# Optimization experiments

Measured on AMD Instinct MI355X. Metric: run time of the kernel, lower is better.

## Reference

```python
import math
import jax, jax.numpy as jnp
import numpy as np

H_HEADS = 8
K_MAX = 64
MIN_WINDOW = 1.0
SHARPNESS = 5.0


def rmsnorm(x, w, eps=1e-6):
    x32 = x.astype(jnp.float32)
    var = jnp.mean(x32 * x32, axis=-1, keepdims=True)
    return (w * (x32 * jax.lax.rsqrt(var + eps))).astype(x.dtype)


def setup_inputs() -> dict:
    key = jax.random.key(0)
    ks = jax.random.split(key, 12)
    B, L, C = 1, 4096, 256
    H, K = H_HEADS, K_MAX
    s = 0.02
    return {
        "x": jax.random.normal(ks[0], (B, L, C), jnp.float32),
        "window_w": jax.random.normal(ks[1], (C, H), jnp.float32) * s,
        "window_b": jnp.zeros((H,), jnp.float32),
        "window_gamma": jnp.ones((H,), jnp.float32),
        "offset_w": jax.random.normal(ks[2], (C, H), jnp.float32) * s,
        "offset_b": jnp.zeros((H,), jnp.float32),
        "offset_gamma": jnp.ones((H,), jnp.float32),
        "kernel_w": jax.random.normal(ks[3], (C, H * K), jnp.float32) * s,
        "kernel_b": jnp.zeros((H * K,), jnp.float32),
        "kernel_gamma": jnp.ones((H * K,), jnp.float32),
        "v_w": jax.random.normal(ks[4], (C, C), jnp.float32) * (1.0 / math.sqrt(C)),
        "v_b": jnp.zeros((C,), jnp.float32),
        "out_w": jax.random.normal(ks[5], (C, C), jnp.float32) * s,
    }


def reference(x, window_w, window_b, window_gamma, offset_w, offset_b, offset_gamma,
              kernel_w, kernel_b, kernel_gamma, v_w, v_b, out_w):
    B, L, C = x.shape
    H, K = H_HEADS, K_MAX
    D = C // H
    max_window = min(int(math.sqrt(L)), K)
    half = max_window // 2
    max_offset = int(math.sqrt(L))
    N = 2 * half + 1  # num_offsets

    # per-position learned window sizes, center offsets, kernel weights
    window_raw = jax.nn.sigmoid(rmsnorm(x @ window_w + window_b, window_gamma))
    window_sizes = MIN_WINDOW + window_raw * (max_window - MIN_WINDOW)      # [B,L,H]
    center_offsets = jnp.tanh(rmsnorm(x @ offset_w + offset_b, offset_gamma)) * max_offset  # [B,L,H]
    kernel_weights = jax.nn.silu(rmsnorm(x @ kernel_w + kernel_b, kernel_gamma)).reshape(B, L, H, K)
    v = (x @ v_w + v_b).reshape(B, L, H, D)

    local = jnp.arange(-half, half + 1, dtype=x.dtype)                      # [N]
    positions = jnp.arange(L, dtype=x.dtype).reshape(1, L, 1, 1)
    neighbor = positions + center_offsets[..., None] + local.reshape(1, 1, 1, N)  # [B,L,H,N]
    valid = (neighbor >= 0) & (neighbor < L)
    nclamp = jnp.clip(neighbor, 0, L - 1)

    rel = jnp.abs(local).reshape(1, 1, 1, N) / (window_sizes[..., None] / 2 + 1e-6)
    window_mask = jax.nn.sigmoid(SHARPNESS * (1.0 - rel)) * valid.astype(x.dtype)

    # kernel interpolation by relative distance
    kidx = jnp.clip(rel, 0, 1) * (K - 1)
    i_fl = jnp.clip(kidx.astype(jnp.int32), 0, K - 2)                       # [B,L,H,N]
    i_ce = i_fl + 1
    w_ce = kidx - i_fl.astype(x.dtype)
    k_fl = jnp.take_along_axis(kernel_weights, i_fl, axis=-1)
    k_ce = jnp.take_along_axis(kernel_weights, i_ce, axis=-1)
    kernel_interp = k_fl * (1.0 - w_ce) + k_ce * w_ce

    attn = kernel_interp * window_mask
    attn = attn / (jnp.sum(attn, axis=-1, keepdims=True) + 1e-6)            # [B,L,H,N]

    # bilinear gather of values at fractional neighbor positions
    p_fl = jnp.clip(jnp.floor(nclamp).astype(jnp.int32), 0, L - 1)
    p_ce = jnp.clip(p_fl + 1, 0, L - 1)
    frac = nclamp - p_fl.astype(x.dtype)                                    # [B,L,H,N]

    v_bh = v.transpose(0, 2, 1, 3)                                          # [B,H,L,D]
    idx_f = p_fl.transpose(0, 2, 1, 3).reshape(B, H, L * N)
    idx_c = p_ce.transpose(0, 2, 1, 3).reshape(B, H, L * N)
    v_fl = jnp.take_along_axis(v_bh, idx_f[..., None], axis=2).reshape(B, H, L, N, D)
    v_ce = jnp.take_along_axis(v_bh, idx_c[..., None], axis=2).reshape(B, H, L, N, D)
    frac_bh = frac.transpose(0, 2, 1, 3)[..., None]                         # [B,H,L,N,1]
    v_nb = v_fl * (1.0 - frac_bh) + v_ce * frac_bh                          # [B,H,L,N,D]

    attn_bh = attn.transpose(0, 2, 1, 3)                                    # [B,H,L,N]
    out = jnp.einsum('bhln,bhlnd->bhld', attn_bh, v_nb)                     # [B,H,L,D]
    out = out.transpose(0, 2, 1, 3).reshape(B, L, C)
    return jax.nn.silu(out @ out_w)
```

## Files before the change

### kernel.cpp

```cpp
#include <hip/hip_runtime.h>
#include <math.h>

#define L_SEQ 4096
#define C_DIM 256
#define H_HEADS 8
#define K_MAX 64
#define D_HEAD 32
#define HALF_W 32
#define N_OFF 65
#define HK 512
#define PW 768

__device__ __forceinline__ float sigmoidf_(float x) { return 1.0f / (1.0f + expf(-x)); }

__global__ void pack_kernel(const float* __restrict__ kw_w, const float* __restrict__ vw,
                            const float* __restrict__ kb, const float* __restrict__ vb,
                            float* __restrict__ Wcat, float* __restrict__ biascat) {
    const int c = blockIdx.x;
    for (int j = threadIdx.x; j < PW; j += 256) {
        Wcat[c * PW + j] = (j < 512) ? kw_w[c * 512 + j] : vw[c * 256 + (j - 512)];
        if (c == 0) biascat[j] = (j < 512) ? kb[j] : vb[j - 512];
    }
}

__global__ void proj_small_kernel(const float* __restrict__ x,
                                  const float* __restrict__ ww, const float* __restrict__ wb,
                                  const float* __restrict__ wg,
                                  const float* __restrict__ ow, const float* __restrict__ ob,
                                  const float* __restrict__ og,
                                  float* __restrict__ wsizes, float* __restrict__ offs) {
    const int l = blockIdx.x;
    const int lane = threadIdx.x;
    const float* xr = x + l * C_DIM;

    float accw[H_HEADS], acco[H_HEADS];
#pragma unroll
    for (int h = 0; h < H_HEADS; ++h) { accw[h] = 0.0f; acco[h] = 0.0f; }

#pragma unroll
    for (int i = 0; i < C_DIM / 64; ++i) {
        const int c = lane + i * 64;
        const float xv = xr[c];
        const float* wwc = ww + c * H_HEADS;
        const float* owc = ow + c * H_HEADS;
#pragma unroll
        for (int h = 0; h < H_HEADS; ++h) {
            accw[h] = fmaf(xv, wwc[h], accw[h]);
            acco[h] = fmaf(xv, owc[h], acco[h]);
        }
    }
#pragma unroll
    for (int off = 32; off > 0; off >>= 1) {
#pragma unroll
        for (int h = 0; h < H_HEADS; ++h) {
            accw[h] += __shfl_xor(accw[h], off);
            acco[h] += __shfl_xor(acco[h], off);
        }
    }
    if (lane == 0) {
        float zw[H_HEADS], zo[H_HEADS];
        float ssw = 0.0f, sso = 0.0f;
#pragma unroll
        for (int h = 0; h < H_HEADS; ++h) {
            zw[h] = accw[h] + wb[h];
            zo[h] = acco[h] + ob[h];
            ssw += zw[h] * zw[h];
            sso += zo[h] * zo[h];
        }
        const float rw = rsqrtf(ssw / (float)H_HEADS + 1e-6f);
        const float ro = rsqrtf(sso / (float)H_HEADS + 1e-6f);
#pragma unroll
        for (int h = 0; h < H_HEADS; ++h) {
            const float nw = wg[h] * zw[h] * rw;
            const float no = og[h] * zo[h] * ro;
            wsizes[l * H_HEADS + h] = 1.0f + sigmoidf_(nw) * 63.0f;
            offs[l * H_HEADS + h]   = tanhf(no) * 64.0f;
        }
    }
}

template <bool ROUTE>
__global__ void gemm_tiled(const float* __restrict__ A, const float* __restrict__ B,
                           const float* __restrict__ biascat, int ldb,
                           float* __restrict__ out,
                           float* __restrict__ kwbuf, float* __restrict__ vbuf) {
    __shared__ float As[16][68];
    __shared__ float Bs[16][68];

    const int tid = threadIdx.x;
    const int tx = tid & 15;
    const int ty = tid >> 4;
    const int l0 = blockIdx.y * 64;
    const int n0 = blockIdx.x * 64;

    const int am = tid >> 2;
    const int ak = (tid & 3) * 4;
    const int bk = tid >> 4;
    const int bn = (tid & 15) * 4;

    float acc[4][4];
#pragma unroll
    for (int i = 0; i < 4; ++i)
#pragma unroll
        for (int j = 0; j < 4; ++j) acc[i][j] = 0.0f;

    for (int k0 = 0; k0 < C_DIM; k0 += 16) {
        const float4 av = *(const float4*)&A[(l0 + am) * C_DIM + k0 + ak];
        const float4 bv = *(const float4*)&B[(k0 + bk) * ldb + n0 + bn];
        __syncthreads();
        As[ak + 0][am] = av.x;
        As[ak + 1][am] = av.y;
        As[ak + 2][am] = av.z;
        As[ak + 3][am] = av.w;
        *(float4*)&Bs[bk][bn] = bv;
        __syncthreads();
#pragma unroll
        for (int kk = 0; kk < 16; ++kk) {
            const float4 a4 = *(const float4*)&As[kk][ty * 4];
            const float4 b4 = *(const float4*)&Bs[kk][tx * 4];
            const float ar[4] = {a4.x, a4.y, a4.z, a4.w};
            const float br[4] = {b4.x, b4.y, b4.z, b4.w};
#pragma unroll
            for (int i = 0; i < 4; ++i)
#pragma unroll
                for (int j = 0; j < 4; ++j)
                    acc[i][j] = fmaf(ar[i], br[j], acc[i][j]);
        }
    }

    const int g0 = n0 + tx * 4;
    if (ROUTE) {
        const float4 bz = *(const float4*)&biascat[g0];
        float* dst;
        int stride, col;
        if (g0 < 512) { dst = kwbuf; stride = 512; col = g0; }
        else          { dst = vbuf;  stride = 256; col = g0 - 512; }
#pragma unroll
        for (int i = 0; i < 4; ++i) {
            const int row = l0 + ty * 4 + i;
            float4 o;
            o.x = acc[i][0] + bz.x;
            o.y = acc[i][1] + bz.y;
            o.z = acc[i][2] + bz.z;
            o.w = acc[i][3] + bz.w;
            *(float4*)&dst[row * stride + col] = o;
        }
    } else {
#pragma unroll
        for (int i = 0; i < 4; ++i) {
            const int row = l0 + ty * 4 + i;
            float4 o;
            o.x = acc[i][0] * sigmoidf_(acc[i][0]);
            o.y = acc[i][1] * sigmoidf_(acc[i][1]);
            o.z = acc[i][2] * sigmoidf_(acc[i][2]);
            o.w = acc[i][3] * sigmoidf_(acc[i][3]);
            *(float4*)&out[row * C_DIM + g0] = o;
        }
    }
}

__global__ void norm_kw(float* __restrict__ kwbuf, const float* __restrict__ kg) {
    const int l = blockIdx.x;
    const int j = threadIdx.x;
    __shared__ float red[256];
    __shared__ float rs_s;
    float* row = kwbuf + l * HK;
    const float z0 = row[j];
    const float z1 = row[j + 256];

    red[j] = z0 * z0 + z1 * z1;
    __syncthreads();
    for (int s = 128; s > 0; s >>= 1) {
        if (j < s) red[j] += red[j + s];
        __syncthreads();
    }
    if (j == 0) rs_s = rsqrtf(red[0] / (float)HK + 1e-6f);
    __syncthreads();
    const float rs = rs_s;

    const float n0 = kg[j] * z0 * rs;
    const float n1 = kg[j + 256] * z1 * rs;
    row[j]       = n0 * sigmoidf_(n0);
    row[j + 256] = n1 * sigmoidf_(n1);
}

__global__ void conv_kernel(const float* __restrict__ wsizes, const float* __restrict__ offs,
                            const float* __restrict__ kw, const float* __restrict__ v,
                            float* __restrict__ out) {
    const int l = blockIdx.x;
    const int tid = threadIdx.x;

    __shared__ float attn[H_HEADS][N_OFF];
    __shared__ int   pfl[H_HEADS][N_OFF];
    __shared__ float frac[H_HEADS][N_OFF];
    __shared__ float inv_denom[H_HEADS];

    for (int t = tid; t < H_HEADS * N_OFF; t += 256) {
        const int h = t / N_OFF;
        const int n = t - h * N_OFF;
        const float ws  = wsizes[l * H_HEADS + h];
        const float off = offs[l * H_HEADS + h];
        const float local = (float)(n - HALF_W);
        const float neighbor = (float)l + off + local;
        const bool valid = (neighbor >= 0.0f) && (neighbor < (float)L_SEQ);
        const float nc = fminf(fmaxf(neighbor, 0.0f), (float)(L_SEQ - 1));

        const float rel = fabsf(local) / (ws * 0.5f + 1e-6f);
        const float mask = sigmoidf_(5.0f * (1.0f - rel)) * (valid ? 1.0f : 0.0f);

        const float kidx = fminf(rel, 1.0f) * (float)(K_MAX - 1);
        int ifl = (int)kidx;
        ifl = min(ifl, K_MAX - 2);
        const float wce = kidx - (float)ifl;
        const float kf = kw[l * HK + h * K_MAX + ifl];
        const float kc = kw[l * HK + h * K_MAX + ifl + 1];
        attn[h][n] = (kf * (1.0f - wce) + kc * wce) * mask;

        int p = (int)floorf(nc);
        p = min(max(p, 0), L_SEQ - 1);
        pfl[h][n] = p;
        frac[h][n] = nc - (float)p;
    }
    __syncthreads();

    if (tid < H_HEADS) {
        float s = 0.0f;
        for (int n = 0; n < N_OFF; ++n) s += attn[tid][n];
        inv_denom[tid] = 1.0f / (s + 1e-6f);
    }
    __syncthreads();

    const int h = tid >> 5;
    const int d = tid & 31;
    float acc = 0.0f;
    for (int n = 0; n < N_OFF; ++n) {
        const float a = attn[h][n];
        const int   p = pfl[h][n];
        const float f = frac[h][n];
        const int  pc = min(p + 1, L_SEQ - 1);
        const float vf = v[p * C_DIM + h * D_HEAD + d];
        const float vc = v[pc * C_DIM + h * D_HEAD + d];
        acc = fmaf(a, vf + f * (vc - vf), acc);
    }
    out[l * C_DIM + h * D_HEAD + d] = acc * inv_denom[h];
}

extern "C" void kernel_launch(void* const* d_in, const int* in_sizes, int n_in,
                              void* d_out, int out_size, void* d_ws, size_t ws_size,
                              hipStream_t stream) {
    const float* x    = (const float*)d_in[0];
    const float* ww   = (const float*)d_in[1];
    const float* wb   = (const float*)d_in[2];
    const float* wg   = (const float*)d_in[3];
    const float* ow   = (const float*)d_in[4];
    const float* ob   = (const float*)d_in[5];
    const float* og   = (const float*)d_in[6];
    const float* kw_w = (const float*)d_in[7];
    const float* kb   = (const float*)d_in[8];
    const float* kg   = (const float*)d_in[9];
    const float* vw   = (const float*)d_in[10];
    const float* vb   = (const float*)d_in[11];
    const float* outw = (const float*)d_in[12];
    float* y = (float*)d_out;

    float* ws_f     = (float*)d_ws;
    float* convbuf  = ws_f;
    float* Wcat     = ws_f;
    float* biascat  = Wcat + 256 * PW;
    float* kwbuf    = convbuf + L_SEQ * C_DIM;
    float* vbuf     = kwbuf + L_SEQ * HK;
    float* wsizes   = vbuf + L_SEQ * C_DIM;
    float* offs     = wsizes + L_SEQ * H_HEADS;

    pack_kernel<<<256, 256, 0, stream>>>(kw_w, vw, kb, vb, Wcat, biascat);
    proj_small_kernel<<<L_SEQ, 64, 0, stream>>>(x, ww, wb, wg, ow, ob, og, wsizes, offs);
    gemm_tiled<true><<<dim3(PW / 64, L_SEQ / 64), 256, 0, stream>>>(
        x, Wcat, biascat, PW, nullptr, kwbuf, vbuf);
    norm_kw<<<L_SEQ, 256, 0, stream>>>(kwbuf, kg);
    conv_kernel<<<L_SEQ, 256, 0, stream>>>(wsizes, offs, kwbuf, vbuf, convbuf);
    gemm_tiled<false><<<dim3(C_DIM / 64, L_SEQ / 64), 256, 0, stream>>>(
        convbuf, outw, nullptr, C_DIM, y, nullptr, nullptr);
}
```

Baseline: 169.5 us.

## Fuse pack, small projections and kw norm into fewer kernels; prefetch GEMM tiles

Removes the weight-packing kernel by having the projection GEMM read the kernel and value weight matrices directly. The small window/offset projection and the kernel-weight RMSNorm+SiLU are folded into the conv kernel, so the normalized row stays in shared memory instead of being written back and re-read. Both GEMMs register-prefetch the next K tile before computing the current one, and the output GEMM uses 32-row tiles to launch more blocks. This cuts the launch count from six to three and removes intermediate global traffic, at the cost of more shared memory and serial prologue work in the conv block.

```diff
diff --git a/kernel.cpp b/kernel.cpp
--- a/kernel.cpp
+++ b/kernel.cpp
@@ -9,81 +9,13 @@
 #define HALF_W 32
 #define N_OFF 65
 #define HK 512
-#define PW 768
 
 __device__ __forceinline__ float sigmoidf_(float x) { return 1.0f / (1.0f + expf(-x)); }
 
-__global__ void pack_kernel(const float* __restrict__ kw_w, const float* __restrict__ vw,
-                            const float* __restrict__ kb, const float* __restrict__ vb,
-                            float* __restrict__ Wcat, float* __restrict__ biascat) {
-    const int c = blockIdx.x;
-    for (int j = threadIdx.x; j < PW; j += 256) {
-        Wcat[c * PW + j] = (j < 512) ? kw_w[c * 512 + j] : vw[c * 256 + (j - 512)];
-        if (c == 0) biascat[j] = (j < 512) ? kb[j] : vb[j - 512];
-    }
-}
-
-__global__ void proj_small_kernel(const float* __restrict__ x,
-                                  const float* __restrict__ ww, const float* __restrict__ wb,
-                                  const float* __restrict__ wg,
-                                  const float* __restrict__ ow, const float* __restrict__ ob,
-                                  const float* __restrict__ og,
-                                  float* __restrict__ wsizes, float* __restrict__ offs) {
-    const int l = blockIdx.x;
-    const int lane = threadIdx.x;
-    const float* xr = x + l * C_DIM;
-
-    float accw[H_HEADS], acco[H_HEADS];
-#pragma unroll
-    for (int h = 0; h < H_HEADS; ++h) { accw[h] = 0.0f; acco[h] = 0.0f; }
-
-#pragma unroll
-    for (int i = 0; i < C_DIM / 64; ++i) {
-        const int c = lane + i * 64;
-        const float xv = xr[c];
-        const float* wwc = ww + c * H_HEADS;
-        const float* owc = ow + c * H_HEADS;
-#pragma unroll
-        for (int h = 0; h < H_HEADS; ++h) {
-            accw[h] = fmaf(xv, wwc[h], accw[h]);
-            acco[h] = fmaf(xv, owc[h], acco[h]);
-        }
-    }
-#pragma unroll
-    for (int off = 32; off > 0; off >>= 1) {
-#pragma unroll
-        for (int h = 0; h < H_HEADS; ++h) {
-            accw[h] += __shfl_xor(accw[h], off);
-            acco[h] += __shfl_xor(acco[h], off);
-        }
-    }
-    if (lane == 0) {
-        float zw[H_HEADS], zo[H_HEADS];
-        float ssw = 0.0f, sso = 0.0f;
-#pragma unroll
-        for (int h = 0; h < H_HEADS; ++h) {
-            zw[h] = accw[h] + wb[h];
-            zo[h] = acco[h] + ob[h];
-            ssw += zw[h] * zw[h];
-            sso += zo[h] * zo[h];
-        }
-        const float rw = rsqrtf(ssw / (float)H_HEADS + 1e-6f);
-        const float ro = rsqrtf(sso / (float)H_HEADS + 1e-6f);
-#pragma unroll
-        for (int h = 0; h < H_HEADS; ++h) {
-            const float nw = wg[h] * zw[h] * rw;
-            const float no = og[h] * zo[h] * ro;
-            wsizes[l * H_HEADS + h] = 1.0f + sigmoidf_(nw) * 63.0f;
-            offs[l * H_HEADS + h]   = tanhf(no) * 64.0f;
-        }
-    }
-}
-
-template <bool ROUTE>
-__global__ void gemm_tiled(const float* __restrict__ A, const float* __restrict__ B,
-                           const float* __restrict__ biascat, int ldb,
-                           float* __restrict__ out,
-                           float* __restrict__ kwbuf, float* __restrict__ vbuf) {
+__global__ void proj_gemm(const float* __restrict__ A, const float* __restrict__ kw_w,
+                          const float* __restrict__ vw, const float* __restrict__ kb,
+                          const float* __restrict__ vb,
+                          float* __restrict__ kwbuf, float* __restrict__ vbuf) {
     __shared__ float As[16][68];
     __shared__ float Bs[16][68];
 
@@ -98,15 +30,21 @@
     const int bk = tid >> 4;
     const int bn = (tid & 15) * 4;
 
+    const float* Bsrc;
+    int ldb, coff;
+    if (n0 < 512) { Bsrc = kw_w; ldb = 512; coff = n0; }
+    else          { Bsrc = vw;   ldb = 256; coff = n0 - 512; }
+
     float acc[4][4];
 #pragma unroll
     for (int i = 0; i < 4; ++i)
 #pragma unroll
-        for (int j = 0; j < 4; ++j) acc[i][j] = 0.0f;
+        for (int jj = 0; jj < 4; ++jj) acc[i][jj] = 0.0f;
+
+    float4 av = *(const float4*)&A[(l0 + am) * C_DIM + ak];
+    float4 bv = *(const float4*)&Bsrc[bk * ldb + coff + bn];
 
     for (int k0 = 0; k0 < C_DIM; k0 += 16) {
-        const float4 av = *(const float4*)&A[(l0 + am) * C_DIM + k0 + ak];
-        const float4 bv = *(const float4*)&B[(k0 + bk) * ldb + n0 + bn];
         __syncthreads();
         As[ak + 0][am] = av.x;
         As[ak + 1][am] = av.y;
@@ -114,6 +52,10 @@
         As[ak + 3][am] = av.w;
         *(float4*)&Bs[bk][bn] = bv;
         __syncthreads();
+        if (k0 + 16 < C_DIM) {
+            av = *(const float4*)&A[(l0 + am) * C_DIM + (k0 + 16) + ak];
+            bv = *(const float4*)&Bsrc[(k0 + 16 + bk) * ldb + coff + bn];
+        }
 #pragma unroll
         for (int kk = 0; kk < 16; ++kk) {
             const float4 a4 = *(const float4*)&As[kk][ty * 4];
@@ -123,83 +65,123 @@
 #pragma unroll
             for (int i = 0; i < 4; ++i)
 #pragma unroll
-                for (int j = 0; j < 4; ++j)
-                    acc[i][j] = fmaf(ar[i], br[j], acc[i][j]);
+                for (int jj = 0; jj < 4; ++jj)
+                    acc[i][jj] = fmaf(ar[i], br[jj], acc[i][jj]);
         }
     }
 
     const int g0 = n0 + tx * 4;
-    if (ROUTE) {
-        const float4 bz = *(const float4*)&biascat[g0];
-        float* dst;
-        int stride, col;
-        if (g0 < 512) { dst = kwbuf; stride = 512; col = g0; }
-        else          { dst = vbuf;  stride = 256; col = g0 - 512; }
-#pragma unroll
-        for (int i = 0; i < 4; ++i) {
-            const int row = l0 + ty * 4 + i;
-            float4 o;
-            o.x = acc[i][0] + bz.x;
-            o.y = acc[i][1] + bz.y;
-            o.z = acc[i][2] + bz.z;
-            o.w = acc[i][3] + bz.w;
-            *(float4*)&dst[row * stride + col] = o;
-        }
-    } else {
-#pragma unroll
-        for (int i = 0; i < 4; ++i) {
-            const int row = l0 + ty * 4 + i;
-            float4 o;
-            o.x = acc[i][0] * sigmoidf_(acc[i][0]);
-            o.y = acc[i][1] * sigmoidf_(acc[i][1]);
-            o.z = acc[i][2] * sigmoidf_(acc[i][2]);
-            o.w = acc[i][3] * sigmoidf_(acc[i][3]);
-            *(float4*)&out[row * C_DIM + g0] = o;
-        }
+    float4 bz;
+    float* dst;
+    int stride, col;
+    if (g0 < 512) { bz = *(const float4*)&kb[g0];       dst = kwbuf; stride = 512; col = g0; }
+    else          { bz = *(const float4*)&vb[g0 - 512]; dst = vbuf;  stride = 256; col = g0 - 512; }
+#pragma unroll
+    for (int i = 0; i < 4; ++i) {
+        const int row = l0 + ty * 4 + i;
+        float4 o;
+        o.x = acc[i][0] + bz.x;
+        o.y = acc[i][1] + bz.y;
+        o.z = acc[i][2] + bz.z;
+        o.w = acc[i][3] + bz.w;
+        *(float4*)&dst[row * stride + col] = o;
     }
 }
 
-__global__ void norm_kw(float* __restrict__ kwbuf, const float* __restrict__ kg) {
+__global__ void conv_fused(const float* __restrict__ x,
+                           const float* __restrict__ ww, const float* __restrict__ wb,
+                           const float* __restrict__ wg,
+                           const float* __restrict__ ow, const float* __restrict__ ob,
+                           const float* __restrict__ og,
+                           const float* __restrict__ kg,
+                           const float* __restrict__ kwraw, const float* __restrict__ v,
+                           float* __restrict__ out) {
     const int l = blockIdx.x;
-    const int j = threadIdx.x;
+    const int tid = threadIdx.x;
+
     __shared__ float red[256];
     __shared__ float rs_s;
-    float* row = kwbuf + l * HK;
-    const float z0 = row[j];
-    const float z1 = row[j + 256];
-
-    red[j] = z0 * z0 + z1 * z1;
-    __syncthreads();
-    for (int s = 128; s > 0; s >>= 1) {
-        if (j < s) red[j] += red[j + s];
-        __syncthreads();
-    }
-    if (j == 0) rs_s = rsqrtf(red[0] / (float)HK + 1e-6f);
-    __syncthreads();
-    const float rs = rs_s;
-
-    const float n0 = kg[j] * z0 * rs;
-    const float n1 = kg[j + 256] * z1 * rs;
-    row[j]       = n0 * sigmoidf_(n0);
-    row[j + 256] = n1 * sigmoidf_(n1);
-}
-
-__global__ void conv_kernel(const float* __restrict__ wsizes, const float* __restrict__ offs,
-                            const float* __restrict__ kw, const float* __restrict__ v,
-                            float* __restrict__ out) {
-    const int l = blockIdx.x;
-    const int tid = threadIdx.x;
-
+    __shared__ float kwrow[HK];
+    __shared__ float wsz[H_HEADS], ofs[H_HEADS];
     __shared__ float attn[H_HEADS][N_OFF];
     __shared__ int   pfl[H_HEADS][N_OFF];
     __shared__ float frac[H_HEADS][N_OFF];
     __shared__ float inv_denom[H_HEADS];
 
+    {
+        const int j = tid;
+        const float* row = kwraw + l * HK;
+        const float z0 = row[j];
+        const float z1 = row[j + 256];
+        red[j] = z0 * z0 + z1 * z1;
+        __syncthreads();
+        for (int s = 128; s > 0; s >>= 1) {
+            if (j < s) red[j] += red[j + s];
+            __syncthreads();
+        }
+        if (j == 0) rs_s = rsqrtf(red[0] / (float)HK + 1e-6f);
+        __syncthreads();
+        const float rs = rs_s;
+        const float n0v = kg[j] * z0 * rs;
+        const float n1v = kg[j + 256] * z1 * rs;
+        kwrow[j]       = n0v * sigmoidf_(n0v);
+        kwrow[j + 256] = n1v * sigmoidf_(n1v);
+    }
+
+    if (tid < 64) {
+        const int lane = tid;
+        const float* xr = x + l * C_DIM;
+        float accw[H_HEADS], acco[H_HEADS];
+#pragma unroll
+        for (int h = 0; h < H_HEADS; ++h) { accw[h] = 0.0f; acco[h] = 0.0f; }
+#pragma unroll
+        for (int i = 0; i < C_DIM / 64; ++i) {
+            const int c = lane + i * 64;
+            const float xv = xr[c];
+            const float* wwc = ww + c * H_HEADS;
+            const float* owc = ow + c * H_HEADS;
+#pragma unroll
+            for (int h = 0; h < H_HEADS; ++h) {
+                accw[h] = fmaf(xv, wwc[h], accw[h]);
+                acco[h] = fmaf(xv, owc[h], acco[h]);
+            }
+        }
+#pragma unroll
+        for (int off = 32; off > 0; off >>= 1) {
+#pragma unroll
+            for (int h = 0; h < H_HEADS; ++h) {
+                accw[h] += __shfl_xor(accw[h], off);
+                acco[h] += __shfl_xor(acco[h], off);
+            }
+        }
+        if (lane == 0) {
+            float zw[H_HEADS], zo[H_HEADS];
+            float ssw = 0.0f, sso = 0.0f;
+#pragma unroll
+            for (int h = 0; h < H_HEADS; ++h) {
+                zw[h] = accw[h] + wb[h];
+                zo[h] = acco[h] + ob[h];
+                ssw += zw[h] * zw[h];
+                sso += zo[h] * zo[h];
+            }
+            const float rw = rsqrtf(ssw / (float)H_HEADS + 1e-6f);
+            const float ro = rsqrtf(sso / (float)H_HEADS + 1e-6f);
+#pragma unroll
+            for (int h = 0; h < H_HEADS; ++h) {
+                const float nw = wg[h] * zw[h] * rw;
+                const float no = og[h] * zo[h] * ro;
+                wsz[h] = 1.0f + sigmoidf_(nw) * 63.0f;
+                ofs[h] = tanhf(no) * 64.0f;
+            }
+        }
+    }
+    __syncthreads();
+
     for (int t = tid; t < H_HEADS * N_OFF; t += 256) {
         const int h = t / N_OFF;
         const int n = t - h * N_OFF;
-        const float ws  = wsizes[l * H_HEADS + h];
-        const float off = offs[l * H_HEADS + h];
+        const float ws  = wsz[h];
+        const float off = ofs[h];
         const float local = (float)(n - HALF_W);
         const float neighbor = (float)l + off + local;
         const bool valid = (neighbor >= 0.0f) && (neighbor < (float)L_SEQ);
@@ -212,8 +194,8 @@
         int ifl = (int)kidx;
         ifl = min(ifl, K_MAX - 2);
         const float wce = kidx - (float)ifl;
-        const float kf = kw[l * HK + h * K_MAX + ifl];
-        const float kc = kw[l * HK + h * K_MAX + ifl + 1];
+        const float kf = kwrow[h * K_MAX + ifl];
+        const float kc = kwrow[h * K_MAX + ifl + 1];
         attn[h][n] = (kf * (1.0f - wce) + kc * wce) * mask;
 
         int p = (int)floorf(nc);
@@ -243,6 +225,74 @@
         acc = fmaf(a, vf + f * (vc - vf), acc);
     }
     out[l * C_DIM + h * D_HEAD + d] = acc * inv_denom[h];
+}
+
+__global__ void out_gemm(const float* __restrict__ A, const float* __restrict__ W,
+                         float* __restrict__ out) {
+    __shared__ float As[16][36];
+    __shared__ float Bs[16][68];
+
+    const int tid = threadIdx.x;
+    const int tx = tid & 15;
+    const int ty = tid >> 4;
+    const int l0 = blockIdx.y * 32;
+    const int n0 = blockIdx.x * 64;
+
+    const int bk = tid >> 4;
+    const int bn = (tid & 15) * 4;
+    const int am = (tid & 127) >> 2;
+    const int ak = (tid & 3) * 4;
+    const bool aload = tid < 128;
+
+    float acc[2][4];
+#pragma unroll
+    for (int i = 0; i < 2; ++i)
+#pragma unroll
+        for (int jj = 0; jj < 4; ++jj) acc[i][jj] = 0.0f;
+
+    float4 av, bv;
+    if (aload) av = *(const float4*)&A[(l0 + am) * C_DIM + ak];
+    bv = *(const float4*)&W[bk * C_DIM + n0 + bn];
+
+    for (int k0 = 0; k0 < C_DIM; k0 += 16) {
+        __syncthreads();
+        if (aload) {
+            As[ak + 0][am] = av.x;
+            As[ak + 1][am] = av.y;
+            As[ak + 2][am] = av.z;
+            As[ak + 3][am] = av.w;
+        }
+        *(float4*)&Bs[bk][bn] = bv;
+        __syncthreads();
+        if (k0 + 16 < C_DIM) {
+            if (aload) av = *(const float4*)&A[(l0 + am) * C_DIM + (k0 + 16) + ak];
+            bv = *(const float4*)&W[(k0 + 16 + bk) * C_DIM + n0 + bn];
+        }
+#pragma unroll
+        for (int kk = 0; kk < 16; ++kk) {
+            const float a0 = As[kk][ty * 2 + 0];
+            const float a1 = As[kk][ty * 2 + 1];
+            const float4 b4 = *(const float4*)&Bs[kk][tx * 4];
+            const float br[4] = {b4.x, b4.y, b4.z, b4.w};
+#pragma unroll
+            for (int jj = 0; jj < 4; ++jj) {
+                acc[0][jj] = fmaf(a0, br[jj], acc[0][jj]);
+                acc[1][jj] = fmaf(a1, br[jj], acc[1][jj]);
+            }
+        }
+    }
+
+    const int g0 = n0 + tx * 4;
+#pragma unroll
+    for (int i = 0; i < 2; ++i) {
+        const int row = l0 + ty * 2 + i;
+        float4 o;
+        o.x = acc[i][0] * sigmoidf_(acc[i][0]);
+        o.y = acc[i][1] * sigmoidf_(acc[i][1]);
+        o.z = acc[i][2] * sigmoidf_(acc[i][2]);
+        o.w = acc[i][3] * sigmoidf_(acc[i][3]);
+        *(float4*)&out[row * C_DIM + g0] = o;
+    }
 }
 
 extern "C" void kernel_launch(void* const* d_in, const int* in_sizes, int n_in,
@@ -263,21 +313,12 @@
     const float* outw = (const float*)d_in[12];
     float* y = (float*)d_out;
 
-    float* ws_f     = (float*)d_ws;
-    float* convbuf  = ws_f;
-    float* Wcat     = ws_f;
-    float* biascat  = Wcat + 256 * PW;
-    float* kwbuf    = convbuf + L_SEQ * C_DIM;
-    float* vbuf     = kwbuf + L_SEQ * HK;
-    float* wsizes   = vbuf + L_SEQ * C_DIM;
-    float* offs     = wsizes + L_SEQ * H_HEADS;
-
-    pack_kernel<<<256, 256, 0, stream>>>(kw_w, vw, kb, vb, Wcat, biascat);
-    proj_small_kernel<<<L_SEQ, 64, 0, stream>>>(x, ww, wb, wg, ow, ob, og, wsizes, offs);
-    gemm_tiled<true><<<dim3(PW / 64, L_SEQ / 64), 256, 0, stream>>>(
-        x, Wcat, biascat, PW, nullptr, kwbuf, vbuf);
-    norm_kw<<<L_SEQ, 256, 0, stream>>>(kwbuf, kg);
-    conv_kernel<<<L_SEQ, 256, 0, stream>>>(wsizes, offs, kwbuf, vbuf, convbuf);
-    gemm_tiled<false><<<dim3(C_DIM / 64, L_SEQ / 64), 256, 0, stream>>>(
-        convbuf, outw, nullptr, C_DIM, y, nullptr, nullptr);
+    float* ws_f    = (float*)d_ws;
+    float* kwbuf   = ws_f;
+    float* vbuf    = kwbuf + L_SEQ * HK;
+    float* convbuf = vbuf + L_SEQ * C_DIM;
+
+    proj_gemm<<<dim3(12, L_SEQ / 64), 256, 0, stream>>>(x, kw_w, vw, kb, vb, kwbuf, vbuf);
+    conv_fused<<<L_SEQ, 256, 0, stream>>>(x, ww, wb, wg, ow, ob, og, kg, kwbuf, vbuf, convbuf);
+    out_gemm<<<dim3(C_DIM / 64, L_SEQ / 32), 256, 0, stream>>>(convbuf, outw, y);
 }
```

New measurement: 163.8 us. -3.4%, faster.
